# Optimization experiments

Hardware: AMD Instinct MI355X
Metric: run time of the kernel (lower is better)

The kernel has to match this reference:

```python
import jax, jax.numpy as jnp
import numpy as np


def setup_inputs() -> dict:
    key = jax.random.key(0)
    B, S, D = 16, 1024, 384
    x = jax.random.normal(jax.random.fold_in(key, 0), (B, S, D), dtype=jnp.float32)
    # integer per-token durations in [0, 10); the layer rounds+casts anyway
    dimensions = jax.random.randint(jax.random.fold_in(key, 1), (B, S), 0, 10).astype(jnp.int32)
    return {"x": x, "dimensions": dimensions}


def reference(x, dimensions):
    # Faithful math of Expand.call: repeat each x[b, i, :] dimensions[b, i] times
    # along axis 1, left-packed, zero-padded to the max total length in the batch.
    dims = jnp.round(dimensions.astype(jnp.float32)).astype(jnp.int32)  # [B, S]
    totals = jnp.sum(dims, axis=1)                                      # [B]
    T = int(jnp.max(totals))  # output length (concrete; matches TF ragged .to_tensor())
    csum = jnp.cumsum(dims, axis=1)                                     # [B, S]
    t = jnp.arange(T, dtype=jnp.int32)                                  # [T]
    # source token index for each output position: first i with csum[i] > t
    idx = jax.vmap(lambda c: jnp.searchsorted(c, t, side='right'))(csum)  # [B, T]
    valid = (t[None, :] < totals[:, None])                              # [B, T]
    idx = jnp.minimum(idx, x.shape[1] - 1)                              # clamp padding positions
    out = jnp.take_along_axis(x, idx[..., None], axis=1)                # [B, T, D] gather
    return out * valid[..., None].astype(x.dtype)
```

## Files before the change

kernel.cpp:

```cpp
#include <hip/hip_runtime.h>
#include <hip/hip_bf16.h>


#define S_TOKENS 1024
#define B_BATCH 16
#define QVEC 96
#define TOK_BLOCKS (B_BATCH * S_TOKENS)
#define PAD_BLOCKS 256

typedef float f4 __attribute__((ext_vector_type(4)));

__global__ void scan_kernel(const int* __restrict__ dims, int* __restrict__ csum) {
    __shared__ int wsum[16];
    __shared__ int wexc[16];
    const int b    = blockIdx.x;
    const int tid  = threadIdx.x;
    const int lane = tid & 63;
    const int wid  = tid >> 6;

    const int v = dims[b * S_TOKENS + tid];
    int inc = v;
#pragma unroll
    for (int d = 1; d < 64; d <<= 1) {
        int u = __shfl_up(inc, d, 64);
        if (lane >= d) inc += u;
    }
    if (lane == 63) wsum[wid] = inc;
    __syncthreads();
    if (tid < 16) {
        int w = wsum[tid];
        int incw = w;
#pragma unroll
        for (int d = 1; d < 16; d <<= 1) {
            int u = __shfl_up(incw, d, 16);
            if (tid >= d) incw += u;
        }
        wexc[tid] = incw - w;
    }
    __syncthreads();
    csum[b * S_TOKENS + tid] = inc + wexc[wid];
}

__global__ __launch_bounds__(64) void expand_kernel(const f4* __restrict__ x4,
                              const int* __restrict__ csum,
                              f4* __restrict__ out4, int T) {
    const int blk = blockIdx.x;
    if (blk < TOK_BLOCKS) {
        const int lane = threadIdx.x;
        const int b    = blk >> 10;
        const int i    = blk & (S_TOKENS - 1);
        const int* __restrict__ c = csum + b * S_TOKENS;
        const int end   = c[i];
        const int start = (i == 0) ? 0 : c[i - 1];
        const int rep   = end - start;
        if (rep <= 0) return;

        const f4* __restrict__ row = x4 + (size_t)(b * S_TOKENS + i) * QVEC;
        f4 v0 = row[lane];
        f4 v1 = (f4)(0.f, 0.f, 0.f, 0.f);
        if (lane < 32) v1 = row[64 + lane];

        f4* dst = out4 + ((size_t)b * T + start) * QVEC;
        for (int r = 0; r < rep; ++r, dst += QVEC) {
            dst[lane] = v0;
            if (lane < 32) dst[64 + lane] = v1;
        }
    } else {
        const int p   = blk - TOK_BLOCKS;
        const int b   = p >> 4;
        const int sub = p & 15;
        const int total = csum[b * S_TOKENS + S_TOKENS - 1];
        const int n = (T - total) * QVEC;
        f4* __restrict__ dst = out4 + ((size_t)b * T + total) * QVEC;
        const f4 z = (f4)(0.f, 0.f, 0.f, 0.f);
        for (int j = sub * 64 + threadIdx.x; j < n; j += 16 * 64)
            dst[j] = z;
    }
}

extern "C" void kernel_launch(void* const* d_in, const int* in_sizes, int n_in,
                              void* d_out, int out_size, void* d_ws, size_t ws_size,
                              hipStream_t stream) {
    const float* x    = (const float*)d_in[0];
    const int*   dims = (const int*)d_in[1];
    float*       out  = (float*)d_out;

    const int D = in_sizes[0] / in_sizes[1];
    const int T = out_size / (B_BATCH * D);

    int* csum = (int*)d_ws;

    scan_kernel<<<B_BATCH, S_TOKENS, 0, stream>>>(dims, csum);

    expand_kernel<<<TOK_BLOCKS + PAD_BLOCKS, 64, 0, stream>>>(
        (const f4*)x, csum, (f4*)out, T);
}
```

Baseline: 140.4 us.

## Fuse prefix-sum scan into expand kernel via per-block redundant reduction

Removes the separate scan kernel and its workspace round trip. Each token block now reads the whole 1024-entry dims row for its batch and computes the prefix sum up to its token with a masked sum and wavefront xor reduction. Padding blocks likewise recompute the row total. This saves one kernel launch and the dependency between the two kernels, at the cost of redundant dims reads (4 KB per block, mostly cache hits) and extra ALU work in every block.

```diff
diff --git a/kernel.cpp b/kernel.cpp
--- a/kernel.cpp
+++ b/kernel.cpp
@@ -9,50 +9,37 @@
 #define PAD_BLOCKS 256
 
 typedef float f4 __attribute__((ext_vector_type(4)));
-
-__global__ void scan_kernel(const int* __restrict__ dims, int* __restrict__ csum) {
-    __shared__ int wsum[16];
-    __shared__ int wexc[16];
-    const int b    = blockIdx.x;
-    const int tid  = threadIdx.x;
-    const int lane = tid & 63;
-    const int wid  = tid >> 6;
-
-    const int v = dims[b * S_TOKENS + tid];
-    int inc = v;
-#pragma unroll
-    for (int d = 1; d < 64; d <<= 1) {
-        int u = __shfl_up(inc, d, 64);
-        if (lane >= d) inc += u;
-    }
-    if (lane == 63) wsum[wid] = inc;
-    __syncthreads();
-    if (tid < 16) {
-        int w = wsum[tid];
-        int incw = w;
-#pragma unroll
-        for (int d = 1; d < 16; d <<= 1) {
-            int u = __shfl_up(incw, d, 16);
-            if (tid >= d) incw += u;
-        }
-        wexc[tid] = incw - w;
-    }
-    __syncthreads();
-    csum[b * S_TOKENS + tid] = inc + wexc[wid];
-}
+typedef int   i4 __attribute__((ext_vector_type(4)));
 
 __global__ __launch_bounds__(64) void expand_kernel(const f4* __restrict__ x4,
-                              const int* __restrict__ csum,
-                              f4* __restrict__ out4, int T) {
-    const int blk = blockIdx.x;
+                                                    const int* __restrict__ dims,
+                                                    f4* __restrict__ out4, int T) {
+    const int blk  = blockIdx.x;
+    const int lane = threadIdx.x;
+
     if (blk < TOK_BLOCKS) {
-        const int lane = threadIdx.x;
-        const int b    = blk >> 10;
-        const int i    = blk & (S_TOKENS - 1);
-        const int* __restrict__ c = csum + b * S_TOKENS;
-        const int end   = c[i];
-        const int start = (i == 0) ? 0 : c[i - 1];
-        const int rep   = end - start;
+        const int b = blk >> 10;
+        const int i = blk & (S_TOKENS - 1);
+        const int* __restrict__ db = dims + b * S_TOKENS;
+        const i4* __restrict__ d4 = (const i4*)db;
+
+        int s_le = 0;
+        const int base = lane * 16;
+#pragma unroll
+        for (int c = 0; c < 4; ++c) {
+            i4 v = d4[lane * 4 + c];
+#pragma unroll
+            for (int e = 0; e < 4; ++e) {
+                int j = base + c * 4 + e;
+                s_le += (j <= i) ? v[e] : 0;
+            }
+        }
+#pragma unroll
+        for (int d = 1; d < 64; d <<= 1)
+            s_le += __shfl_xor(s_le, d, 64);
+
+        const int rep   = db[i];
+        const int start = s_le - rep;
         if (rep <= 0) return;
 
         const f4* __restrict__ row = x4 + (size_t)(b * S_TOKENS + i) * QVEC;
@@ -69,11 +56,23 @@
         const int p   = blk - TOK_BLOCKS;
         const int b   = p >> 4;
         const int sub = p & 15;
-        const int total = csum[b * S_TOKENS + S_TOKENS - 1];
+        const i4* __restrict__ d4 = (const i4*)(dims + b * S_TOKENS);
+
+        int s_all = 0;
+#pragma unroll
+        for (int c = 0; c < 4; ++c) {
+            i4 v = d4[lane * 4 + c];
+            s_all += v[0] + v[1] + v[2] + v[3];
+        }
+#pragma unroll
+        for (int d = 1; d < 64; d <<= 1)
+            s_all += __shfl_xor(s_all, d, 64);
+
+        const int total = s_all;
         const int n = (T - total) * QVEC;
         f4* __restrict__ dst = out4 + ((size_t)b * T + total) * QVEC;
         const f4 z = (f4)(0.f, 0.f, 0.f, 0.f);
-        for (int j = sub * 64 + threadIdx.x; j < n; j += 16 * 64)
+        for (int j = sub * 64 + lane; j < n; j += 16 * 64)
             dst[j] = z;
     }
 }
@@ -88,10 +87,6 @@
     const int D = in_sizes[0] / in_sizes[1];
     const int T = out_size / (B_BATCH * D);
 
-    int* csum = (int*)d_ws;
-
-    scan_kernel<<<B_BATCH, S_TOKENS, 0, stream>>>(dims, csum);
-
     expand_kernel<<<TOK_BLOCKS + PAD_BLOCKS, 64, 0, stream>>>(
-        (const f4*)x, csum, (f4*)out, T);
+        (const f4*)x, dims, (f4*)out, T);
 }
```

Result: no change. 140.2 us (-0.1%).
